# Kernel optimization log

Measured on AMD Instinct MI355X. Metric: run time of the kernel, lower is better.

The kernel has to match this reference:

```python
import math
import jax, jax.numpy as jnp
import numpy as np

B, T, D, H = 2, 2048, 1024, 16  # batch, max_T, d_model, heads
DK = D // H


def setup_inputs() -> dict:
    key = jax.random.key(0)
    ks = jax.random.split(key, 5)
    scale = 1.0 / math.sqrt(D)
    return {
        "k": jax.random.normal(ks[0], (B, T, D), jnp.float32),
        "q": jax.random.normal(ks[1], (B, T, D), jnp.float32),
        "v": jax.random.normal(ks[2], (B, T, D), jnp.float32),
        "mask": jnp.ones((B, T), jnp.int32),
        "causal": 1,
        # Single shared Linear: the torch code binds the SAME nn.Linear to K/Q/V/out.
        "W": jax.random.uniform(ks[3], (D, D), jnp.float32, -scale, scale),
        "b": jax.random.uniform(ks[4], (D,), jnp.float32, -scale, scale),
    }


def reference(k, q, v, mask, causal, W, b):
    def proj(x):  # [B,T,D] -> [B,H,T,DK]
        return (x @ W.T + b).reshape(B, T, H, DK).transpose(0, 2, 1, 3)

    K, Q, V = proj(k), proj(q), proj(v)
    scores = jnp.einsum("bhqd,bhkd->bhqk", Q, K) / math.sqrt(DK)
    if causal:
        causal_mask = jnp.tril(jnp.ones((T, T), jnp.bool_))[None, None]
        scores = jnp.where(causal_mask, scores, -jnp.inf)
    # outer-product padding mask: [B,T] -> [B,1,T,T]
    m = mask.astype(jnp.float32)
    mm = (m[:, None, :, None] * m[:, None, None, :])  # [B,1,T,T]
    scores = jnp.where(mm == 0, -jnp.inf, scores)
    p = jax.nn.softmax(scores, axis=-1)  # dropout is identity in eval
    out = jnp.einsum("bhqk,bhkd->bhqd", p, V)  # [B,H,T,DK]
    concat = out.transpose(0, 2, 1, 3).reshape(B, T, D)
    return concat @ W.T + b
```

## Files before the change

### kernel.cpp

```cpp
#include <hip/hip_runtime.h>

#define TT 2048
#define DD 1024
#define HH 16
#define DKK 64
#define BB 2

typedef __attribute__((ext_vector_type(8))) short bf16x8;
typedef __attribute__((ext_vector_type(4))) short bf16x4;
typedef __attribute__((ext_vector_type(4))) float f32x4;
typedef __attribute__((ext_vector_type(4))) unsigned short us4;

__device__ __forceinline__ unsigned short f2bf(float f) {
  union { float f; unsigned int i; } v; v.f = f;
  unsigned int x = v.i;
  return (unsigned short)((x + 0x7fffu + ((x >> 16) & 1u)) >> 16);
}
__device__ __forceinline__ unsigned int cvtpk_bf16(float lo, float hi) {
  unsigned int r;
  asm("v_cvt_pk_bf16_f32 %0, %1, %2" : "=v"(r) : "v"(lo), "v"(hi));
  return r;
}
__device__ __forceinline__ void gload16(const void* g, void* l) {
  __builtin_amdgcn_global_load_lds((const __attribute__((address_space(1))) void*)g,
                                   (__attribute__((address_space(3))) void*)l,
                                   16, 0, 0);
}

#if defined(__has_builtin)
#if __has_builtin(__builtin_amdgcn_exp2f)
#define HAVE_EXP2 1
#endif
#if __has_builtin(__builtin_amdgcn_mfma_f32_16x16x16bf16_1k)
#define HAVE_MFMA16 1
#endif
#endif

__device__ __forceinline__ float fexp2(float x) {
#ifdef HAVE_EXP2
  return __builtin_amdgcn_exp2f(x);
#else
  return __builtin_exp2f(x);
#endif
}

__device__ __forceinline__ f32x4 mfma16(bf16x4 a, bf16x4 b, f32x4 c) {
#ifdef HAVE_MFMA16
  return __builtin_amdgcn_mfma_f32_16x16x16bf16_1k(a, b, c, 0, 0, 0);
#else
  asm volatile("v_mfma_f32_16x16x16_bf16 %0, %1, %2, %0\n\ts_nop 7\n\ts_nop 7"
               : "+v"(c) : "v"(a), "v"(b));
  return c;
#endif
}

__global__ __launch_bounds__(256)
void f2b_all(const float* __restrict__ k, const float* __restrict__ q,
             const float* __restrict__ v, const float* __restrict__ W,
             unsigned short* __restrict__ kb, unsigned short* __restrict__ qb,
             unsigned short* __restrict__ vb, unsigned short* __restrict__ Wb)
{
  const int n1 = (BB * TT * DD) / 4;
  const int nW = (DD * DD) / 4;
  const int total = 3 * n1 + nW;
  int i = blockIdx.x * 256 + threadIdx.x;
  const int stride = gridDim.x * 256;
  for (; i < total; i += stride) {
    const float* src; unsigned short* dst; int j = i;
    if (j < n1)            { src = k; dst = kb; }
    else if (j < 2 * n1)   { src = q; dst = qb; j -= n1; }
    else if (j < 3 * n1)   { src = v; dst = vb; j -= 2 * n1; }
    else                   { src = W; dst = Wb; j -= 3 * n1; }
    const float4 f = ((const float4*)src)[j];
    us4 o;
    o[0] = f2bf(f.x); o[1] = f2bf(f.y); o[2] = f2bf(f.z); o[3] = f2bf(f.w);
    ((us4*)dst)[j] = o;
  }
}


__global__ __launch_bounds__(256)
void gemm_proj(const unsigned short* __restrict__ kb, const unsigned short* __restrict__ qb,
               const unsigned short* __restrict__ vb, const unsigned short* __restrict__ W,
               const float* __restrict__ bias,
               unsigned short* __restrict__ Kp, unsigned short* __restrict__ Qp,
               unsigned short* __restrict__ Vt)
{
  __shared__ unsigned short lA[2][128 * 32];
  __shared__ unsigned short lB[2][64 * 32];
  const int tid = threadIdx.x;
  const int w = tid >> 6, l = tid & 63;
  const int hw = blockIdx.y * gridDim.x + blockIdx.x;
  const int virt = (hw & 7) * 192 + (hw >> 3);
  const int n0 = (virt & 15) * 64;
  const int my = virt >> 4;
  const int grp = my >> 5;
  const int m0 = (my & 31) * 128;
  const unsigned short* A = grp == 0 ? kb : (grp == 1 ? qb : vb);
  const int wr = w >> 1, wc = w & 1;
  const int lg = l >> 4, lc = l & 15;

  f32x4 acc[4][2];
#pragma unroll
  for (int i = 0; i < 4; ++i)
#pragma unroll
    for (int j = 0; j < 2; ++j) acc[i][j] = (f32x4){0.f, 0.f, 0.f, 0.f};

  const int scolb = (((l & 3) ^ ((l >> 2) & 3)) * 16);

  auto stage = [&](int buf, int k0) {
#pragma unroll
    for (int cc = 0; cc < 2; ++cc) {
      const int slot = w * 2 + cc;
      const int row = slot * 16 + (l >> 2);
      gload16(A + (size_t)(m0 + row) * DD + k0 + (scolb >> 1), &lA[buf][slot * 512]);
    }
    {
      const int row = w * 16 + (l >> 2);
      gload16(W + (size_t)(n0 + row) * DD + k0 + (scolb >> 1), &lB[buf][w * 512]);
    }
  };

  stage(0, 0);
  __syncthreads();
  int cur = 0;
#pragma unroll 1
  for (int kt = 0; kt < 32; ++kt) {
    if (kt < 31) stage(cur ^ 1, (kt + 1) * 32);
    const char* la = (const char*)lA[cur];
    const char* lb = (const char*)lB[cur];
    bf16x8 af[4], bfr[2];
#pragma unroll
    for (int mf = 0; mf < 4; ++mf)
      af[mf] = *(const bf16x8*)(la + (wr * 64 + mf * 16 + lc) * 64 + ((lg * 16) ^ ((lc & 3) << 4)));
#pragma unroll
    for (int nf = 0; nf < 2; ++nf)
      bfr[nf] = *(const bf16x8*)(lb + (wc * 32 + nf * 16 + lc) * 64 + ((lg * 16) ^ ((lc & 3) << 4)));
#pragma unroll
    for (int mf = 0; mf < 4; ++mf)
#pragma unroll
      for (int nf = 0; nf < 2; ++nf)
        acc[mf][nf] = __builtin_amdgcn_mfma_f32_16x16x32_bf16(af[mf], bfr[nf], acc[mf][nf], 0, 0, 0);
    __syncthreads();
    cur ^= 1;
  }

  const float scale = (grp == 1) ? 0.125f * 1.4426950408889634f : 1.0f;
#pragma unroll
  for (int nf = 0; nf < 2; ++nf) {
    const int colg = n0 + wc * 32 + nf * 16 + lc;
    const float bv = bias[colg];
#pragma unroll
    for (int mf = 0; mf < 4; ++mf) {
      const int rowg = m0 + wr * 64 + mf * 16 + lg * 4;
      if (grp < 2) {
        unsigned short* C = grp == 0 ? Kp : Qp;
#pragma unroll
        for (int r = 0; r < 4; ++r)
          C[(size_t)(rowg + r) * DD + colg] = f2bf(scale * (acc[mf][nf][r] + bv));
      } else {
        const int bb = rowg >> 11, t = rowg & (TT - 1);
        const int hh = colg >> 6, dk = colg & 63;
        us4 pk;
#pragma unroll
        for (int r = 0; r < 4; ++r) pk[r] = f2bf(acc[mf][nf][r] + bv);
        *(us4*)&Vt[((size_t)((bb * HH + hh) * DKK + dk)) * TT + t] = pk;
      }
    }
  }
}

__global__ __launch_bounds__(256)
void gemm_out(const unsigned short* __restrict__ A, const unsigned short* __restrict__ W,
              const float* __restrict__ bias, float* __restrict__ Cf)
{
  __shared__ unsigned short lA[2][64 * 32];
  __shared__ unsigned short lB[2][64 * 32];
  const int tid = threadIdx.x;
  const int w = tid >> 6, l = tid & 63;
  const int hw = blockIdx.y * gridDim.x + blockIdx.x;
  const int virt = (hw & 7) * 128 + (hw >> 3);
  const int n0 = (virt & 15) * 64, m0 = (virt >> 4) * 64;
  const int wr = w >> 1, wc = w & 1;
  const int lg = l >> 4, lc = l & 15;

  f32x4 acc[2][2];
#pragma unroll
  for (int i = 0; i < 2; ++i)
#pragma unroll
    for (int j = 0; j < 2; ++j) acc[i][j] = (f32x4){0.f, 0.f, 0.f, 0.f};

  const int scolb = (((l & 3) ^ ((l >> 2) & 3)) * 16);

  auto stage = [&](int buf, int k0) {
    const int row = w * 16 + (l >> 2);
    gload16(A + (size_t)(m0 + row) * DD + k0 + (scolb >> 1), &lA[buf][w * 512]);
    gload16(W + (size_t)(n0 + row) * DD + k0 + (scolb >> 1), &lB[buf][w * 512]);
  };

  stage(0, 0);
  __syncthreads();
  int cur = 0;
#pragma unroll 1
  for (int kt = 0; kt < 32; ++kt) {
    if (kt < 31) stage(cur ^ 1, (kt + 1) * 32);
    const char* la = (const char*)lA[cur];
    const char* lb = (const char*)lB[cur];
    bf16x8 af[2], bfr[2];
#pragma unroll
    for (int mf = 0; mf < 2; ++mf)
      af[mf] = *(const bf16x8*)(la + (wr * 32 + mf * 16 + lc) * 64 + ((lg * 16) ^ ((lc & 3) << 4)));
#pragma unroll
    for (int nf = 0; nf < 2; ++nf)
      bfr[nf] = *(const bf16x8*)(lb + (wc * 32 + nf * 16 + lc) * 64 + ((lg * 16) ^ ((lc & 3) << 4)));
#pragma unroll
    for (int mf = 0; mf < 2; ++mf)
#pragma unroll
      for (int nf = 0; nf < 2; ++nf)
        acc[mf][nf] = __builtin_amdgcn_mfma_f32_16x16x32_bf16(af[mf], bfr[nf], acc[mf][nf], 0, 0, 0);
    __syncthreads();
    cur ^= 1;
  }

#pragma unroll
  for (int nf = 0; nf < 2; ++nf) {
    const int colg = n0 + wc * 32 + nf * 16 + lc;
    const float bv = bias[colg];
#pragma unroll
    for (int mf = 0; mf < 2; ++mf) {
      const int rowg = m0 + wr * 32 + mf * 16 + lg * 4;
#pragma unroll
      for (int r = 0; r < 4; ++r)
        Cf[(size_t)(rowg + r) * DD + colg] = acc[mf][nf][r] + bv;
    }
  }
}

__global__ __launch_bounds__(256)
void attn(const unsigned short* __restrict__ Qp,
          const unsigned short* __restrict__ Kp,
          const unsigned short* __restrict__ Vt,
          const int* __restrict__ maskp,
          const int* __restrict__ causalp,
          unsigned short* __restrict__ Oc)
{
  __shared__ unsigned short Kl[2][64 * 64];
  __shared__ unsigned short Vl[2][64 * 64];
  const int tid = threadIdx.x;
  const int w = tid >> 6, l = tid & 63;
  const int bh = blockIdx.x;
  const int q0 = (31 - blockIdx.y) * 64;
  const int b = bh >> 4, h = bh & 15;
  const int lg = l >> 4, lc = l & 15;
  const int causal = causalp[0];
  const int qr = q0 + w * 16 + lc;

  bf16x8 qf[2];
  {
    const unsigned short* qp = Qp + (size_t)(b * TT + qr) * DD + h * DKK + lg * 8;
    qf[0] = *(const bf16x8*)qp;
    qf[1] = *(const bf16x8*)(qp + 32);
  }
  f32x4 o[4];
#pragma unroll
  for (int nfo = 0; nfo < 4; ++nfo) o[nfo] = (f32x4){0.f, 0.f, 0.f, 0.f};
  float m = -1e30f, lsum = 0.f;

  const int swz = ((l & 7) ^ (l >> 3)) * 16;
  int kcoff[2], vcoff[4];
#pragma unroll
  for (int kk = 0; kk < 2; ++kk) kcoff[kk] = (kk * 64 + lg * 16) ^ ((lc & 7) << 4);
#pragma unroll
  for (int nfk = 0; nfk < 4; ++nfk) vcoff[nfk] = (nfk * 32 + lg * 8) ^ ((lc & 7) << 4);
  const int rowb = lc * 128;
  const int* mrow = maskp + b * TT;

  auto stage = [&](int buf, int c0) {
#pragma unroll
    for (int cc = 0; cc < 2; ++cc) {
      const int slot = w * 2 + cc;
      const int rr = slot * 8 + (l >> 3);
      gload16(Kp + (size_t)(b * TT + c0 + rr) * DD + h * DKK + (swz >> 1), &Kl[buf][slot * 512]);
      gload16(Vt + (size_t)((b * HH + h) * DKK + rr) * TT + c0 + (swz >> 1), &Vl[buf][slot * 512]);
    }
  };

  const int ntiles = (causal ? (q0 + 64) : TT) >> 6;
  stage(0, 0);
  __syncthreads();
  int cur = 0;
#pragma unroll 1
  for (int t = 0; t < ntiles; ++t) {
    if (t + 1 < ntiles) stage(cur ^ 1, (t + 1) * 64);
    const int c0 = t * 64;
    const char* kl = (const char*)Kl[cur];
    const char* vl = (const char*)Vl[cur];

    f32x4 s[4];
#pragma unroll
    for (int nf = 0; nf < 4; ++nf) s[nf] = (f32x4){0.f, 0.f, 0.f, 0.f};
#pragma unroll
    for (int nf = 0; nf < 4; ++nf)
#pragma unroll
      for (int kk = 0; kk < 2; ++kk) {
        bf16x8 kf = *(const bf16x8*)(kl + rowb + kcoff[kk] + nf * 2048);
        s[nf] = __builtin_amdgcn_mfma_f32_16x16x32_bf16(kf, qf[kk], s[nf], 0, 0, 0);
      }

    const unsigned long long bal = __ballot(mrow[c0 + l] != 0);
    if (bal != ~0ull) {
#pragma unroll
      for (int nf = 0; nf < 4; ++nf) {
        const int4 mv = *(const int4*)&mrow[c0 + nf * 16 + lg * 4];
        const int mvr[4] = {mv.x, mv.y, mv.z, mv.w};
#pragma unroll
        for (int r = 0; r < 4; ++r)
          if (mvr[r] == 0) s[nf][r] = -1e30f;
      }
    }
    if (causal && (t == ntiles - 1)) {
#pragma unroll
      for (int nf = 0; nf < 4; ++nf)
#pragma unroll
        for (int r = 0; r < 4; ++r) {
          const int kg = c0 + nf * 16 + lg * 4 + r;
          if (kg > qr) s[nf][r] = -1e30f;
        }
    }

    float pm = fmaxf(fmaxf(fmaxf(s[0][0], s[0][1]), fmaxf(s[0][2], s[0][3])),
                     fmaxf(fmaxf(s[1][0], s[1][1]), fmaxf(s[1][2], s[1][3])));
    pm = fmaxf(pm, fmaxf(fmaxf(fmaxf(s[2][0], s[2][1]), fmaxf(s[2][2], s[2][3])),
                         fmaxf(fmaxf(s[3][0], s[3][1]), fmaxf(s[3][2], s[3][3]))));
    pm = fmaxf(pm, __shfl_xor(pm, 16, 64));
    pm = fmaxf(pm, __shfl_xor(pm, 32, 64));

    if (!__all((m > -1e28f) && (pm <= m + 8.0f))) {
      const float mn = fmaxf(fmaxf(m, pm), -1e28f);
      const float al = fexp2(m - mn);
      m = mn;
      float alr[4];
#pragma unroll
      for (int r = 0; r < 4; ++r) alr[r] = __shfl(al, lg * 4 + r, 64);
#pragma unroll
      for (int nfo = 0; nfo < 4; ++nfo)
#pragma unroll
        for (int r = 0; r < 4; ++r) o[nfo][r] *= alr[r];
      lsum *= al;
    }

    float ps = 0.f;
    bf16x4 pa[4];
#pragma unroll
    for (int nf = 0; nf < 4; ++nf) {
      const float p0 = fexp2(s[nf][0] - m);
      const float p1 = fexp2(s[nf][1] - m);
      const float p2 = fexp2(s[nf][2] - m);
      const float p3 = fexp2(s[nf][3] - m);
      ps += (p0 + p1) + (p2 + p3);
      union { unsigned int u[2]; bf16x4 v; } pk;
      pk.u[0] = cvtpk_bf16(p0, p1);
      pk.u[1] = cvtpk_bf16(p2, p3);
      pa[nf] = pk.v;
    }
    lsum += ps;

#pragma unroll
    for (int nfo = 0; nfo < 4; ++nfo)
#pragma unroll
      for (int nfk = 0; nfk < 4; ++nfk) {
        bf16x4 vb = *(const bf16x4*)(vl + rowb + vcoff[nfk] + nfo * 2048);
        o[nfo] = mfma16(pa[nfk], vb, o[nfo]);
      }

    __syncthreads();
    cur ^= 1;
  }

  lsum += __shfl_xor(lsum, 16, 64);
  lsum += __shfl_xor(lsum, 32, 64);
  float linv[4];
#pragma unroll
  for (int r = 0; r < 4; ++r) linv[r] = 1.0f / __shfl(lsum, lg * 4 + r, 64);
#pragma unroll
  for (int nfo = 0; nfo < 4; ++nfo) {
    const int dg = h * DKK + nfo * 16 + lc;
#pragma unroll
    for (int r = 0; r < 4; ++r) {
      const int qg = q0 + w * 16 + lg * 4 + r;
      Oc[(size_t)(b * TT + qg) * DD + dg] = f2bf(o[nfo][r] * linv[r]);
    }
  }
}

extern "C" void kernel_launch(void* const* d_in, const int* in_sizes, int n_in,
                              void* d_out, int out_size, void* d_ws, size_t ws_size,
                              hipStream_t stream)
{
  (void)in_sizes; (void)n_in; (void)out_size; (void)ws_size;
  const float* kf = (const float*)d_in[0];
  const float* qf = (const float*)d_in[1];
  const float* vf = (const float*)d_in[2];
  const int* mask = (const int*)d_in[3];
  const int* causal = (const int*)d_in[4];
  const float* Wf = (const float*)d_in[5];
  const float* bf = (const float*)d_in[6];

  const size_t MB = 1024 * 1024;
  char* ws = (char*)d_ws;
  unsigned short* kb = (unsigned short*)(ws);
  unsigned short* qb = (unsigned short*)(ws + 8 * MB);
  unsigned short* vb = (unsigned short*)(ws + 16 * MB);
  unsigned short* Wb = (unsigned short*)(ws + 24 * MB);
  unsigned short* Kp = (unsigned short*)(ws + 26 * MB);
  unsigned short* Qp = (unsigned short*)(ws + 34 * MB);
  unsigned short* Vt = (unsigned short*)(ws + 42 * MB);
  unsigned short* Oc = kb;

  f2b_all<<<dim3(2048), dim3(256), 0, stream>>>(kf, qf, vf, Wf, kb, qb, vb, Wb);
  gemm_proj<<<dim3(16, 96), dim3(256), 0, stream>>>(kb, qb, vb, Wb, bf, Kp, Qp, Vt);
  attn<<<dim3(32, 32), dim3(256), 0, stream>>>(Qp, Kp, Vt, mask, causal, Oc);
  gemm_out<<<dim3(16, 64), dim3(256), 0, stream>>>(Oc, Wb, bf, (float*)d_out);
}
```

Before: 127.6 us.

## Fuse fp32-to-bf16 input conversion into projection GEMM A-tile loading

The separate conversion pass over k, q and v is removed. The projection GEMM now loads fp32 activations straight into registers, packs them to bf16 with v_cvt_pk_bf16_f32, and writes them into swizzled LDS after the MFMAs, double-buffered against compute. Only W is still pre-converted by a small kernel. This avoids writing and re-reading 24 MB of bf16 intermediates. The cost is twice the global read bytes per A tile inside the GEMM, plus extra register pressure and VALU work in the main loop.

```diff
diff --git a/kernel.cpp b/kernel.cpp
--- a/kernel.cpp
+++ b/kernel.cpp
@@ -10,6 +10,7 @@
 typedef __attribute__((ext_vector_type(4))) short bf16x4;
 typedef __attribute__((ext_vector_type(4))) float f32x4;
 typedef __attribute__((ext_vector_type(4))) unsigned short us4;
+typedef __attribute__((ext_vector_type(4))) unsigned int u32x4;
 
 __device__ __forceinline__ unsigned short f2bf(float f) {
   union { float f; unsigned int i; } v; v.f = f;
@@ -55,33 +56,23 @@
 }
 
 __global__ __launch_bounds__(256)
-void f2b_all(const float* __restrict__ k, const float* __restrict__ q,
-             const float* __restrict__ v, const float* __restrict__ W,
-             unsigned short* __restrict__ kb, unsigned short* __restrict__ qb,
-             unsigned short* __restrict__ vb, unsigned short* __restrict__ Wb)
+void f2bW(const float* __restrict__ in, unsigned short* __restrict__ out)
 {
-  const int n1 = (BB * TT * DD) / 4;
-  const int nW = (DD * DD) / 4;
-  const int total = 3 * n1 + nW;
+  const int n4 = (DD * DD) / 4;
   int i = blockIdx.x * 256 + threadIdx.x;
   const int stride = gridDim.x * 256;
-  for (; i < total; i += stride) {
-    const float* src; unsigned short* dst; int j = i;
-    if (j < n1)            { src = k; dst = kb; }
-    else if (j < 2 * n1)   { src = q; dst = qb; j -= n1; }
-    else if (j < 3 * n1)   { src = v; dst = vb; j -= 2 * n1; }
-    else                   { src = W; dst = Wb; j -= 3 * n1; }
-    const float4 f = ((const float4*)src)[j];
+  for (; i < n4; i += stride) {
+    const float4 f = ((const float4*)in)[i];
     us4 o;
     o[0] = f2bf(f.x); o[1] = f2bf(f.y); o[2] = f2bf(f.z); o[3] = f2bf(f.w);
-    ((us4*)dst)[j] = o;
+    ((us4*)out)[i] = o;
   }
 }
 
 
 __global__ __launch_bounds__(256)
-void gemm_proj(const unsigned short* __restrict__ kb, const unsigned short* __restrict__ qb,
-               const unsigned short* __restrict__ vb, const unsigned short* __restrict__ W,
+void gemm_proj(const float* __restrict__ kf, const float* __restrict__ qf,
+               const float* __restrict__ vf, const unsigned short* __restrict__ W,
                const float* __restrict__ bias,
                unsigned short* __restrict__ Kp, unsigned short* __restrict__ Qp,
                unsigned short* __restrict__ Vt)
@@ -96,7 +87,7 @@
   const int my = virt >> 4;
   const int grp = my >> 5;
   const int m0 = (my & 31) * 128;
-  const unsigned short* A = grp == 0 ? kb : (grp == 1 ? qb : vb);
+  const float* A = grp == 0 ? kf : (grp == 1 ? qf : vf);
   const int wr = w >> 1, wc = w & 1;
   const int lg = l >> 4, lc = l & 15;
 
@@ -108,25 +99,47 @@
 
   const int scolb = (((l & 3) ^ ((l >> 2) & 3)) * 16);
 
-  auto stage = [&](int buf, int k0) {
-#pragma unroll
-    for (int cc = 0; cc < 2; ++cc) {
-      const int slot = w * 2 + cc;
-      const int row = slot * 16 + (l >> 2);
-      gload16(A + (size_t)(m0 + row) * DD + k0 + (scolb >> 1), &lA[buf][slot * 512]);
-    }
-    {
-      const int row = w * 16 + (l >> 2);
-      gload16(W + (size_t)(n0 + row) * DD + k0 + (scolb >> 1), &lB[buf][w * 512]);
-    }
+  const int arow0 = (w * 2 + 0) * 16 + (l >> 2);
+  const int arow1 = (w * 2 + 1) * 16 + (l >> 2);
+  const int asl = l & 3;
+  const int adst0 = arow0 * 64 + ((asl * 16) ^ ((arow0 & 3) << 4));
+  const int adst1 = arow1 * 64 + ((asl * 16) ^ ((arow1 & 3) << 4));
+
+  float4 areg[4];
+  auto issueA = [&](int k0) {
+    const float* s0 = A + (size_t)(m0 + arow0) * DD + k0 + asl * 8;
+    const float* s1 = A + (size_t)(m0 + arow1) * DD + k0 + asl * 8;
+    areg[0] = *(const float4*)s0;
+    areg[1] = *(const float4*)(s0 + 4);
+    areg[2] = *(const float4*)s1;
+    areg[3] = *(const float4*)(s1 + 4);
   };
-
-  stage(0, 0);
+  auto writeA = [&](int buf) {
+    u32x4 p0, p1;
+    p0[0] = cvtpk_bf16(areg[0].x, areg[0].y);
+    p0[1] = cvtpk_bf16(areg[0].z, areg[0].w);
+    p0[2] = cvtpk_bf16(areg[1].x, areg[1].y);
+    p0[3] = cvtpk_bf16(areg[1].z, areg[1].w);
+    p1[0] = cvtpk_bf16(areg[2].x, areg[2].y);
+    p1[1] = cvtpk_bf16(areg[2].z, areg[2].w);
+    p1[2] = cvtpk_bf16(areg[3].x, areg[3].y);
+    p1[3] = cvtpk_bf16(areg[3].z, areg[3].w);
+    *(u32x4*)((char*)lA[buf] + adst0) = p0;
+    *(u32x4*)((char*)lA[buf] + adst1) = p1;
+  };
+  auto stageB = [&](int buf, int k0) {
+    const int row = w * 16 + (l >> 2);
+    gload16(W + (size_t)(n0 + row) * DD + k0 + (scolb >> 1), &lB[buf][w * 512]);
+  };
+
+  issueA(0);
+  stageB(0, 0);
+  writeA(0);
   __syncthreads();
   int cur = 0;
 #pragma unroll 1
   for (int kt = 0; kt < 32; ++kt) {
-    if (kt < 31) stage(cur ^ 1, (kt + 1) * 32);
+    if (kt < 31) { issueA((kt + 1) * 32); stageB(cur ^ 1, (kt + 1) * 32); }
     const char* la = (const char*)lA[cur];
     const char* lb = (const char*)lB[cur];
     bf16x8 af[4], bfr[2];
@@ -141,6 +154,7 @@
 #pragma unroll
       for (int nf = 0; nf < 2; ++nf)
         acc[mf][nf] = __builtin_amdgcn_mfma_f32_16x16x32_bf16(af[mf], bfr[nf], acc[mf][nf], 0, 0, 0);
+    if (kt < 31) writeA(cur ^ 1);
     __syncthreads();
     cur ^= 1;
   }
@@ -408,17 +422,14 @@
 
   const size_t MB = 1024 * 1024;
   char* ws = (char*)d_ws;
-  unsigned short* kb = (unsigned short*)(ws);
-  unsigned short* qb = (unsigned short*)(ws + 8 * MB);
-  unsigned short* vb = (unsigned short*)(ws + 16 * MB);
-  unsigned short* Wb = (unsigned short*)(ws + 24 * MB);
-  unsigned short* Kp = (unsigned short*)(ws + 26 * MB);
-  unsigned short* Qp = (unsigned short*)(ws + 34 * MB);
-  unsigned short* Vt = (unsigned short*)(ws + 42 * MB);
-  unsigned short* Oc = kb;
-
-  f2b_all<<<dim3(2048), dim3(256), 0, stream>>>(kf, qf, vf, Wf, kb, qb, vb, Wb);
-  gemm_proj<<<dim3(16, 96), dim3(256), 0, stream>>>(kb, qb, vb, Wb, bf, Kp, Qp, Vt);
+  unsigned short* Wb = (unsigned short*)(ws);
+  unsigned short* Kp = (unsigned short*)(ws + 2 * MB);
+  unsigned short* Qp = (unsigned short*)(ws + 10 * MB);
+  unsigned short* Vt = (unsigned short*)(ws + 18 * MB);
+  unsigned short* Oc = (unsigned short*)(ws + 26 * MB);
+
+  f2bW<<<dim3(512), dim3(256), 0, stream>>>(Wf, Wb);
+  gemm_proj<<<dim3(16, 96), dim3(256), 0, stream>>>(kf, qf, vf, Wb, bf, Kp, Qp, Vt);
   attn<<<dim3(32, 32), dim3(256), 0, stream>>>(Qp, Kp, Vt, mask, causal, Oc);
   gemm_out<<<dim3(16, 64), dim3(256), 0, stream>>>(Oc, Wb, bf, (float*)d_out);
 }
```

New measurement: 143.2 us. +12.3%, slower.
